# Kernel tuning notes

Measured on AMD Instinct MI355X. Metric: run time of the kernel, lower is better.

The kernel has to match this reference:

```python
import jax, jax.numpy as jnp
import numpy as np

D = 1024        # model dim
H = 8           # num heads
HD = D // H     # head dim = 128
EPS = 1e-6
B, L = 2, 4096


def _rmsnorm(x, g):
    # RMSNorm over the full model dim (applied before head split, as in source)
    return x * jax.lax.rsqrt(jnp.mean(x * x, axis=-1, keepdims=True) + EPS) * g


def _rope_interleaved(x, cos, sin):
    # x: [B, L, H, HD]; cos/sin: [L, HD//2]
    x1 = x[..., 0::2]
    x2 = x[..., 1::2]
    c = cos[None, :, None, :]
    s = sin[None, :, None, :]
    # interleave (x1*c - x2*s, x1*s + x2*c) back into even/odd lanes
    out = jnp.stack([x1 * c - x2 * s, x1 * s + x2 * c], axis=-1)
    return out.reshape(x.shape)


def setup_inputs() -> dict:
    key = jax.random.key(0)
    ks = jax.random.split(key, 6)
    x = jax.random.normal(ks[0], (B, L, D), dtype=jnp.float32)
    freqs_cos = jax.random.uniform(ks[1], (L, HD // 2), dtype=jnp.float32)
    freqs_sin = jax.random.uniform(ks[2], (L, HD // 2), dtype=jnp.float32)
    s = 1.0 / np.sqrt(D).astype(np.float32)
    w_qkv = jax.random.normal(ks[3], (D, 3 * D), dtype=jnp.float32) * s
    b_qkv = jnp.zeros((3 * D,), dtype=jnp.float32)
    g_q = jnp.ones((D,), dtype=jnp.float32)
    g_k = jnp.ones((D,), dtype=jnp.float32)
    w_out = jax.random.normal(ks[4], (D, D), dtype=jnp.float32) * s
    b_out = jnp.zeros((D,), dtype=jnp.float32)
    return {"x": x, "freqs_cos": freqs_cos, "freqs_sin": freqs_sin,
            "w_qkv": w_qkv, "b_qkv": b_qkv, "g_q": g_q, "g_k": g_k,
            "w_out": w_out, "b_out": b_out}


def reference(x, freqs_cos, freqs_sin, w_qkv, b_qkv, g_q, g_k, w_out, b_out):
    Bx, Lx, _ = x.shape
    qkv = x @ w_qkv + b_qkv                      # [B, L, 3D]
    q, k, v = jnp.split(qkv, 3, axis=-1)          # each [B, L, D]
    q = _rmsnorm(q, g_q)
    k = _rmsnorm(k, g_k)
    q = q.reshape(Bx, Lx, H, HD)
    k = k.reshape(Bx, Lx, H, HD)
    v = v.reshape(Bx, Lx, H, HD)
    q = _rope_interleaved(q, freqs_cos, freqs_sin)
    k = _rope_interleaved(k, freqs_cos, freqs_sin)
    scale = 1.0 / np.sqrt(HD)
    scores = jnp.einsum('blhd,bmhd->bhlm', q, k) * scale
    attn = jax.nn.softmax(scores, axis=-1)
    o = jnp.einsum('bhlm,bmhd->blhd', attn, v).reshape(Bx, Lx, D)
    return o @ w_out + b_out
```

## Files before the change

kernel.cpp:

```cpp
#include <hip/hip_runtime.h>
#include <hip/hip_bf16.h>
#include <stdint.h>

typedef __attribute__((ext_vector_type(8))) short short8;
typedef __attribute__((ext_vector_type(4))) short short4v;
typedef __attribute__((ext_vector_type(4))) float f32x4;
typedef __attribute__((ext_vector_type(16))) float f32x16;

#define LSEQ 4096
#define DMODEL 1024
#define NHEAD 8
#define HDIM 128
#define MTOT 8192
#define NQKV 3072

__device__ __forceinline__ unsigned short f2bf(float f){
  unsigned u = __float_as_uint(f);
  u += 0x7fffu + ((u >> 16) & 1u);
  return (unsigned short)(u >> 16);
}
__device__ __forceinline__ float bf2f(unsigned short h){
  return __uint_as_float(((unsigned)h) << 16);
}

typedef const __attribute__((address_space(1))) void* gas_ptr;
typedef __attribute__((address_space(3))) void* las_ptr;
__device__ __forceinline__ void gload_lds16(const void* g, void* l){
  __builtin_amdgcn_global_load_lds((gas_ptr)(uintptr_t)g,
                                   (las_ptr)(unsigned)(uintptr_t)l, 16, 0, 0);
}

__global__ __launch_bounds__(256) void k_cvt(const float* __restrict__ in,
                                             unsigned short* __restrict__ out, int n8){
  int i = blockIdx.x*256 + threadIdx.x;
  if (i >= n8) return;
  const float4* p = (const float4*)in + (size_t)i*2;
  float4 a = p[0], b = p[1];
  short8 r;
  r[0]=(short)f2bf(a.x); r[1]=(short)f2bf(a.y); r[2]=(short)f2bf(a.z); r[3]=(short)f2bf(a.w);
  r[4]=(short)f2bf(b.x); r[5]=(short)f2bf(b.y); r[6]=(short)f2bf(b.z); r[7]=(short)f2bf(b.w);
  *(short8*)(out + (size_t)i*8) = r;
}

__global__ __launch_bounds__(256) void k_transpose_cvt(const float* __restrict__ in,
                                                       unsigned short* __restrict__ out,
                                                       int R, int C){
  __shared__ unsigned short tile[32][33];
  int c0 = blockIdx.x*32, r0 = blockIdx.y*32;
  int tx = threadIdx.x & 31, ty = threadIdx.x >> 5;
  #pragma unroll
  for (int i=0;i<32;i+=8)
    tile[ty+i][tx] = f2bf(in[(size_t)(r0+ty+i)*C + c0+tx]);
  __syncthreads();
  #pragma unroll
  for (int i=0;i<32;i+=8)
    out[(size_t)(c0+ty+i)*R + r0+tx] = tile[tx][ty+i];
}

__global__ __launch_bounds__(256) void k_vT(const unsigned short* __restrict__ qkv,
                                            unsigned short* __restrict__ vT){
  __shared__ unsigned short tile[32][33];
  int bh = blockIdx.z; int b = bh >> 3, h = bh & 7;
  int l0 = blockIdx.x*32, d0 = blockIdx.y*32;
  const unsigned short* src = qkv + (size_t)b*LSEQ*NQKV + 2*DMODEL + h*HDIM;
  int tx = threadIdx.x & 31, ty = threadIdx.x >> 5;
  #pragma unroll
  for (int i=0;i<32;i+=8)
    tile[ty+i][tx] = src[(size_t)(l0+ty+i)*NQKV + d0+tx];
  __syncthreads();
  unsigned short* dst = vT + ((size_t)bh*HDIM + d0)*LSEQ + l0;
  #pragma unroll
  for (int i=0;i<32;i+=8)
    dst[(size_t)(ty+i)*LSEQ + tx] = tile[tx][ty+i];
}

template<int OUT_BF16>
__global__ __launch_bounds__(256) void k_gemm_bt(const unsigned short* __restrict__ A,
                                                 const unsigned short* __restrict__ Bt,
                                                 const float* __restrict__ bias,
                                                 void* __restrict__ Cout,
                                                 int M, int N, int K){
  __shared__ unsigned short As[128*64];
  __shared__ unsigned short Bs[128*64];
  int tid = threadIdx.x, lane = tid & 63, wave = tid >> 6;
  int wm = wave >> 1, wn = wave & 1;
  int nbx = N >> 7;
  int nwg = nbx * (M >> 7);
  int id  = blockIdx.y * nbx + blockIdx.x;
  int cpx = nwg >> 3;
  int swz = (id & 7) * cpx + (id >> 3);
  int m0 = (swz / nbx) * 128, n0 = (swz % nbx) * 128;
  f32x4 zero = {0.f,0.f,0.f,0.f};
  f32x4 acc[4][4];
  #pragma unroll
  for (int mi=0;mi<4;++mi)
    #pragma unroll
    for (int ni=0;ni<4;++ni) acc[mi][ni] = zero;

  int srow = lane >> 3;
  int soffb = (lane & 7) * 16;
  int scol = (soffb ^ (srow << 4)) >> 1;
  int cg = lane >> 4, cl = lane & 15;

  int nkt = K >> 6;
  for (int kt = 0; kt < nkt; ++kt){
    if (kt) __syncthreads();
    int kbase = kt*64;
    #pragma unroll
    for (int j=0;j<4;++j){
      int ch = wave*4 + j;
      int row = ch*8 + srow;
      gload_lds16(A  + (size_t)(m0+row)*K + kbase + scol, (char*)As + ch*1024);
      gload_lds16(Bt + (size_t)(n0+row)*K + kbase + scol, (char*)Bs + ch*1024);
    }
    __syncthreads();

    short8 af[4][2], bf[4][2];
    #pragma unroll
    for (int mi=0;mi<4;++mi){
      int row = wm*64 + mi*16 + cl;
      int key = (row & 7) << 4;
      #pragma unroll
      for (int kk=0;kk<2;++kk)
        af[mi][kk] = *(const short8*)((const char*)As + row*128 + ((kk*64 + cg*16) ^ key));
    }
    #pragma unroll
    for (int ni=0;ni<4;++ni){
      int row = wn*64 + ni*16 + cl;
      int key = (row & 7) << 4;
      #pragma unroll
      for (int kk=0;kk<2;++kk)
        bf[ni][kk] = *(const short8*)((const char*)Bs + row*128 + ((kk*64 + cg*16) ^ key));
    }
    #pragma unroll
    for (int kk=0;kk<2;++kk)
      #pragma unroll
      for (int mi=0;mi<4;++mi)
        #pragma unroll
        for (int ni=0;ni<4;++ni)
          acc[mi][ni] = __builtin_amdgcn_mfma_f32_16x16x32_bf16(af[mi][kk], bf[ni][kk], acc[mi][ni], 0,0,0);
  }

  #pragma unroll
  for (int ni=0;ni<4;++ni){
    int col = n0 + wn*64 + ni*16 + cl;
    float bv = bias[col];
    #pragma unroll
    for (int mi=0;mi<4;++mi){
      int r = m0 + wm*64 + mi*16 + cg*4;
      #pragma unroll
      for (int i=0;i<4;++i){
        float v = acc[mi][ni][i] + bv;
        if (OUT_BF16) ((unsigned short*)Cout)[(size_t)(r+i)*N + col] = f2bf(v);
        else          ((float*)Cout)[(size_t)(r+i)*N + col] = v;
      }
    }
  }
}

__global__ __launch_bounds__(256) void k_norm_rope(unsigned short* __restrict__ qkv,
                                                   const float* __restrict__ fcos,
                                                   const float* __restrict__ fsin,
                                                   const float* __restrict__ gq,
                                                   const float* __restrict__ gk){
  int bl = blockIdx.x;
  int l = bl & (LSEQ-1);
  int t = threadIdx.x;
  unsigned short* row = qkv + (size_t)bl * NQKV;
  int d0 = t*4;
  short4v qv = *(short4v*)(row + d0);
  short4v kv = *(short4v*)(row + DMODEL + d0);
  float q[4], k[4];
  #pragma unroll
  for (int j=0;j<4;++j){ q[j] = bf2f((unsigned short)qv[j]); k[j] = bf2f((unsigned short)kv[j]); }
  float sq = q[0]*q[0]+q[1]*q[1]+q[2]*q[2]+q[3]*q[3];
  float sk = k[0]*k[0]+k[1]*k[1]+k[2]*k[2]+k[3]*k[3];
  #pragma unroll
  for (int o=32;o;o>>=1){ sq += __shfl_xor(sq,o); sk += __shfl_xor(sk,o); }
  __shared__ float red[8];
  int lane = t & 63, wv = t >> 6;
  if (!lane){ red[wv] = sq; red[4+wv] = sk; }
  __syncthreads();
  sq = red[0]+red[1]+red[2]+red[3];
  sk = red[4]+red[5]+red[6]+red[7];
  const float K2 = 0.12753568849800323f;
  float rq = rsqrtf(sq*(1.f/1024.f) + 1e-6f);
  float rk = rsqrtf(sk*(1.f/1024.f) + 1e-6f) * K2;
  int hd = d0 & (HDIM-1);
  int fi = (l << 6) + (hd >> 1);
  float c0 = fcos[fi], s0 = fsin[fi], c1 = fcos[fi+1], s1 = fsin[fi+1];
  {
    float x1 = q[0]*rq*gq[d0],   x2 = q[1]*rq*gq[d0+1];
    float x3 = q[2]*rq*gq[d0+2], x4 = q[3]*rq*gq[d0+3];
    short4v qo;
    qo[0]=(short)f2bf(x1*c0 - x2*s0); qo[1]=(short)f2bf(x1*s0 + x2*c0);
    qo[2]=(short)f2bf(x3*c1 - x4*s1); qo[3]=(short)f2bf(x3*s1 + x4*c1);
    *(short4v*)(row + d0) = qo;
  }
  {
    float x1 = k[0]*rk*gk[d0],   x2 = k[1]*rk*gk[d0+1];
    float x3 = k[2]*rk*gk[d0+2], x4 = k[3]*rk*gk[d0+3];
    short4v ko;
    ko[0]=(short)f2bf(x1*c0 - x2*s0); ko[1]=(short)f2bf(x1*s0 + x2*c0);
    ko[2]=(short)f2bf(x3*c1 - x4*s1); ko[3]=(short)f2bf(x3*s1 + x4*c1);
    *(short4v*)(row + DMODEL + d0) = ko;
  }
}

__global__ __launch_bounds__(256, 2) void k_attn(const unsigned short* __restrict__ qkv,
                                                 const unsigned short* __restrict__ vT,
                                                 unsigned short* __restrict__ o){
  __shared__ unsigned short Ks[2][64*128];
  __shared__ unsigned short VTs[2][128*64];
  int bh = blockIdx.y; int b = bh >> 3, h = bh & 7;
  int q0 = blockIdx.x * 128;
  int tid = threadIdx.x, lane = tid & 63, wave = tid >> 6;
  int ql = lane & 31, hf = lane >> 5;
  const unsigned short* base = qkv + (size_t)b*LSEQ*NQKV + h*HDIM;
  const unsigned short* kgl = base + DMODEL;
  const unsigned short* vtg = vT + (size_t)bh*HDIM*LSEQ;

  short8 qf[8];
  {
    const unsigned short* qr = base + (size_t)(q0 + wave*32 + ql)*NQKV + hf*8;
    #pragma unroll
    for (int st=0;st<8;++st) qf[st] = *(const short8*)(qr + st*16);
  }
  short8 ones;
  #pragma unroll
  for (int j=0;j<8;++j) ones[j] = (short)0x3F80;

  f32x16 z16 = {0.f};
  f32x16 acc[4];
  acc[0]=z16; acc[1]=z16; acc[2]=z16; acc[3]=z16;
  f32x16 accl = z16;

  int key = (ql & 7) << 4;

  int v_dl   = lane >> 3;
  int v_srcb = ((lane & 7)*16) ^ (v_dl << 4);
  int cgk = (lane >> 4) & 3;

  const unsigned short* kptr[4];
  const unsigned short* vptr[4];
  #pragma unroll
  for (int j=0;j<4;++j){
    int ch = wave*4 + j;
    int row = ch*4 + cgk;
    int srcb = ((lane & 15)*16) ^ ((row & 7) << 4);
    kptr[j] = kgl + (size_t)row*NQKV + (srcb >> 1);
    int d = ch*8 + v_dl;
    vptr[j] = vtg + (size_t)d*LSEQ + (v_srcb >> 1);
    gload_lds16(kptr[j], (char*)Ks[0] + ch*1024);
    gload_lds16(vptr[j], (char*)VTs[0] + ch*1024);
    kptr[j] += 64*NQKV;
    vptr[j] += 64;
  }

  const int NT = LSEQ/64;
  for (int t = 0; t < NT; ++t){
    int cur = t & 1;
    __syncthreads();

    if (t+1 < NT){
      #pragma unroll
      for (int j=0;j<4;++j){
        int ch = wave*4 + j;
        gload_lds16(kptr[j], (char*)Ks[cur^1] + ch*1024);
        gload_lds16(vptr[j], (char*)VTs[cur^1] + ch*1024);
        kptr[j] += 64*NQKV;
        vptr[j] += 64;
      }
    }

    const char* kb = (const char*)Ks[cur];
    const char* vb = (const char*)VTs[cur];

    __builtin_amdgcn_s_setprio(1);
    f32x16 s0 = z16, s1 = z16;
    #pragma unroll
    for (int st=0;st<8;++st){
      int col = (hf*16 + st*32) ^ key;
      short8 kf0 = *(const short8*)(kb + ql*256 + col);
      s0 = __builtin_amdgcn_mfma_f32_32x32x16_bf16(kf0, qf[st], s0, 0,0,0);
    }
    #pragma unroll
    for (int st=0;st<8;++st){
      int col = (hf*16 + st*32) ^ key;
      short8 kf1 = *(const short8*)(kb + ql*256 + 8192 + col);
      s1 = __builtin_amdgcn_mfma_f32_32x32x16_bf16(kf1, qf[st], s1, 0,0,0);
      s0[2*st]   = __builtin_amdgcn_exp2f(s0[2*st]);
      s0[2*st+1] = __builtin_amdgcn_exp2f(s0[2*st+1]);
    }
    #pragma unroll
    for (int c=0;c<2;++c){
      unsigned c01, c23, c45, c67;
      int rb = c*8;
      asm("v_cvt_pk_bf16_f32 %0, %1, %2" : "=v"(c01) : "v"(s0[rb+0]), "v"(s0[rb+1]));
      asm("v_cvt_pk_bf16_f32 %0, %1, %2" : "=v"(c23) : "v"(s0[rb+2]), "v"(s0[rb+3]));
      asm("v_cvt_pk_bf16_f32 %0, %1, %2" : "=v"(c45) : "v"(s0[rb+4]), "v"(s0[rb+5]));
      asm("v_cvt_pk_bf16_f32 %0, %1, %2" : "=v"(c67) : "v"(s0[rb+6]), "v"(s0[rb+7]));
      asm("v_permlane32_swap_b32 %0, %1" : "+v"(c01), "+v"(c45));
      asm("v_permlane32_swap_b32 %0, %1" : "+v"(c23), "+v"(c67));
      union { unsigned u[4]; short8 v; } pu;
      pu.u[0] = c01; pu.u[1] = c23; pu.u[2] = c45; pu.u[3] = c67;
      short8 pa = pu.v;
      s1[rb+0] = __builtin_amdgcn_exp2f(s1[rb+0]);
      s1[rb+1] = __builtin_amdgcn_exp2f(s1[rb+1]);
      s1[rb+2] = __builtin_amdgcn_exp2f(s1[rb+2]);
      s1[rb+3] = __builtin_amdgcn_exp2f(s1[rb+3]);
      s1[rb+4] = __builtin_amdgcn_exp2f(s1[rb+4]);
      s1[rb+5] = __builtin_amdgcn_exp2f(s1[rb+5]);
      s1[rb+6] = __builtin_amdgcn_exp2f(s1[rb+6]);
      s1[rb+7] = __builtin_amdgcn_exp2f(s1[rb+7]);
      accl = __builtin_amdgcn_mfma_f32_32x32x16_bf16(pa, ones, accl, 0,0,0);
      #pragma unroll
      for (int dt=0;dt<4;++dt){
        int col = (c*32 + hf*16) ^ key;
        short8 vf = *(const short8*)(vb + (dt*32 + ql)*128 + col);
        acc[dt] = __builtin_amdgcn_mfma_f32_32x32x16_bf16(pa, vf, acc[dt], 0,0,0);
      }
    }
    #pragma unroll
    for (int c=2;c<4;++c){
      unsigned c01, c23, c45, c67;
      int rb = (c&1)*8;
      asm("v_cvt_pk_bf16_f32 %0, %1, %2" : "=v"(c01) : "v"(s1[rb+0]), "v"(s1[rb+1]));
      asm("v_cvt_pk_bf16_f32 %0, %1, %2" : "=v"(c23) : "v"(s1[rb+2]), "v"(s1[rb+3]));
      asm("v_cvt_pk_bf16_f32 %0, %1, %2" : "=v"(c45) : "v"(s1[rb+4]), "v"(s1[rb+5]));
      asm("v_cvt_pk_bf16_f32 %0, %1, %2" : "=v"(c67) : "v"(s1[rb+6]), "v"(s1[rb+7]));
      asm("v_permlane32_swap_b32 %0, %1" : "+v"(c01), "+v"(c45));
      asm("v_permlane32_swap_b32 %0, %1" : "+v"(c23), "+v"(c67));
      union { unsigned u[4]; short8 v; } pu;
      pu.u[0] = c01; pu.u[1] = c23; pu.u[2] = c45; pu.u[3] = c67;
      short8 pa = pu.v;
      accl = __builtin_amdgcn_mfma_f32_32x32x16_bf16(pa, ones, accl, 0,0,0);
      #pragma unroll
      for (int dt=0;dt<4;++dt){
        int col = (c*32 + hf*16) ^ key;
        short8 vf = *(const short8*)(vb + (dt*32 + ql)*128 + col);
        acc[dt] = __builtin_amdgcn_mfma_f32_32x32x16_bf16(pa, vf, acc[dt], 0,0,0);
      }
    }
    __builtin_amdgcn_s_setprio(0);
  }

  float rr[16];
  #pragma unroll
  for (int r=0;r<16;++r) rr[r] = __builtin_amdgcn_rcpf(accl[r]);
  size_t qbase = (size_t)(b*LSEQ + q0 + wave*32);
  #pragma unroll
  for (int dt=0;dt<4;++dt){
    int col = h*HDIM + dt*32 + ql;
    #pragma unroll
    for (int r=0;r<16;++r){
      int qrow = (r&3) + 8*(r>>2) + 4*hf;
      o[(qbase + qrow)*DMODEL + col] = f2bf(acc[dt][r]*rr[r]);
    }
  }
}

extern "C" void kernel_launch(void* const* d_in, const int* in_sizes, int n_in,
                              void* d_out, int out_size, void* d_ws, size_t ws_size,
                              hipStream_t stream) {
  const float* x    = (const float*)d_in[0];
  const float* fcos = (const float*)d_in[1];
  const float* fsin = (const float*)d_in[2];
  const float* wqkv = (const float*)d_in[3];
  const float* bqkv = (const float*)d_in[4];
  const float* gq   = (const float*)d_in[5];
  const float* gk   = (const float*)d_in[6];
  const float* wout = (const float*)d_in[7];
  const float* bout = (const float*)d_in[8];
  float* out = (float*)d_out;

  char* ws = (char*)d_ws;
  unsigned short* xb    = (unsigned short*)(ws);
  unsigned short* qkv   = (unsigned short*)(ws + (16ull<<20));
  unsigned short* ob    = (unsigned short*)(ws + (64ull<<20));
  unsigned short* wqkvT = (unsigned short*)(ws + (80ull<<20));
  unsigned short* woutT = (unsigned short*)(ws + (86ull<<20));
  unsigned short* vT    = xb;

  k_cvt<<<4096, 256, 0, stream>>>(x, xb, (MTOT*DMODEL)/8);
  k_transpose_cvt<<<dim3(96,32), 256, 0, stream>>>(wqkv, wqkvT, DMODEL, NQKV);
  k_transpose_cvt<<<dim3(32,32), 256, 0, stream>>>(wout, woutT, DMODEL, DMODEL);
  k_gemm_bt<1><<<dim3(NQKV/128, MTOT/128), 256, 0, stream>>>(xb, wqkvT, bqkv, qkv, MTOT, NQKV, DMODEL);
  k_norm_rope<<<MTOT, 256, 0, stream>>>(qkv, fcos, fsin, gq, gk);
  k_vT<<<dim3(LSEQ/32, HDIM/32, 16), 256, 0, stream>>>(qkv, vT);
  k_attn<<<dim3(LSEQ/128, 16), 256, 0, stream>>>(qkv, vT, ob);
  k_gemm_bt<0><<<dim3(DMODEL/128, MTOT/128), 256, 0, stream>>>(ob, woutT, bout, out, MTOT, DMODEL, DMODEL);
}
```

Measured before the change: 259.6 us.

## Double-buffer GEMM LDS tiles with 256x128 blocks of 8 waves

Replaces the 128x128 single-buffered GEMM with a 256x128 tile run by 512 threads. A and B tiles are double-buffered in LDS, and the next K-slice is prefetched while the current one is computed, using explicit vmcnt waits and barriers. MFMA sections get a raised wave priority. The aim is to hide global-load latency and halve the B-tile reloads per output row. In exchange, LDS use rises to 96KB and occupancy drops to one block per CU, and the out-projection grid shrinks to 256 blocks.

```diff
diff --git a/kernel.cpp b/kernel.cpp
--- a/kernel.cpp
+++ b/kernel.cpp
@@ -75,21 +75,22 @@
 }
 
 template<int OUT_BF16>
-__global__ __launch_bounds__(256) void k_gemm_bt(const unsigned short* __restrict__ A,
-                                                 const unsigned short* __restrict__ Bt,
-                                                 const float* __restrict__ bias,
-                                                 void* __restrict__ Cout,
-                                                 int M, int N, int K){
-  __shared__ unsigned short As[128*64];
-  __shared__ unsigned short Bs[128*64];
+__global__ __launch_bounds__(512, 1) void k_gemm256(const unsigned short* __restrict__ A,
+                                                    const unsigned short* __restrict__ Bt,
+                                                    const float* __restrict__ bias,
+                                                    void* __restrict__ Cout,
+                                                    int M, int N, int K){
+  __shared__ unsigned short As[2][256*64];
+  __shared__ unsigned short Bs[2][128*64];
   int tid = threadIdx.x, lane = tid & 63, wave = tid >> 6;
   int wm = wave >> 1, wn = wave & 1;
   int nbx = N >> 7;
-  int nwg = nbx * (M >> 7);
+  int nwg = nbx * (M >> 8);
   int id  = blockIdx.y * nbx + blockIdx.x;
   int cpx = nwg >> 3;
   int swz = (id & 7) * cpx + (id >> 3);
-  int m0 = (swz / nbx) * 128, n0 = (swz % nbx) * 128;
+  int m0 = (swz / nbx) * 256, n0 = (swz % nbx) * 128;
+
   f32x4 zero = {0.f,0.f,0.f,0.f};
   f32x4 acc[4][4];
   #pragma unroll
@@ -98,23 +99,51 @@
     for (int ni=0;ni<4;++ni) acc[mi][ni] = zero;
 
   int srow = lane >> 3;
-  int soffb = (lane & 7) * 16;
-  int scol = (soffb ^ (srow << 4)) >> 1;
+  int scol = (((lane & 7)*16) ^ (srow << 4)) >> 1;
   int cg = lane >> 4, cl = lane & 15;
 
-  int nkt = K >> 6;
-  for (int kt = 0; kt < nkt; ++kt){
-    if (kt) __syncthreads();
-    int kbase = kt*64;
-    #pragma unroll
-    for (int j=0;j<4;++j){
-      int ch = wave*4 + j;
-      int row = ch*8 + srow;
-      gload_lds16(A  + (size_t)(m0+row)*K + kbase + scol, (char*)As + ch*1024);
-      gload_lds16(Bt + (size_t)(n0+row)*K + kbase + scol, (char*)Bs + ch*1024);
-    }
-    __syncthreads();
-
+  const int NT2 = K >> 6;
+  #pragma unroll
+  for (int j=0;j<4;++j){
+    int ch = wave*4 + j;
+    int row = ch*8 + srow;
+    gload_lds16(A + (size_t)(m0+row)*K + scol, (char*)As[0] + ch*1024);
+  }
+  #pragma unroll
+  for (int j=0;j<2;++j){
+    int ch = wave*2 + j;
+    int row = ch*8 + srow;
+    gload_lds16(Bt + (size_t)(n0+row)*K + scol, (char*)Bs[0] + ch*1024);
+  }
+
+  for (int kt = 0; kt < NT2; ++kt){
+    int cur = kt & 1;
+    __builtin_amdgcn_s_barrier();
+    __builtin_amdgcn_sched_barrier(0);
+    if (kt+1 < NT2){
+      int kbase = (kt+1)*64;
+      #pragma unroll
+      for (int j=0;j<4;++j){
+        int ch = wave*4 + j;
+        int row = ch*8 + srow;
+        gload_lds16(A + (size_t)(m0+row)*K + kbase + scol, (char*)As[cur^1] + ch*1024);
+      }
+      #pragma unroll
+      for (int j=0;j<2;++j){
+        int ch = wave*2 + j;
+        int row = ch*8 + srow;
+        gload_lds16(Bt + (size_t)(n0+row)*K + kbase + scol, (char*)Bs[cur^1] + ch*1024);
+      }
+      asm volatile("s_waitcnt vmcnt(6)" ::: "memory");
+    } else {
+      asm volatile("s_waitcnt vmcnt(0)" ::: "memory");
+    }
+    __builtin_amdgcn_sched_barrier(0);
+    __builtin_amdgcn_s_barrier();
+    __builtin_amdgcn_sched_barrier(0);
+
+    const char* ab = (const char*)As[cur];
+    const char* bb = (const char*)Bs[cur];
     short8 af[4][2], bf[4][2];
     #pragma unroll
     for (int mi=0;mi<4;++mi){
@@ -122,7 +151,7 @@
       int key = (row & 7) << 4;
       #pragma unroll
       for (int kk=0;kk<2;++kk)
-        af[mi][kk] = *(const short8*)((const char*)As + row*128 + ((kk*64 + cg*16) ^ key));
+        af[mi][kk] = *(const short8*)(ab + row*128 + ((kk*64 + cg*16) ^ key));
     }
     #pragma unroll
     for (int ni=0;ni<4;++ni){
@@ -130,8 +159,9 @@
       int key = (row & 7) << 4;
       #pragma unroll
       for (int kk=0;kk<2;++kk)
-        bf[ni][kk] = *(const short8*)((const char*)Bs + row*128 + ((kk*64 + cg*16) ^ key));
-    }
+        bf[ni][kk] = *(const short8*)(bb + row*128 + ((kk*64 + cg*16) ^ key));
+    }
+    __builtin_amdgcn_s_setprio(1);
     #pragma unroll
     for (int kk=0;kk<2;++kk)
       #pragma unroll
@@ -139,6 +169,7 @@
         #pragma unroll
         for (int ni=0;ni<4;++ni)
           acc[mi][ni] = __builtin_amdgcn_mfma_f32_16x16x32_bf16(af[mi][kk], bf[ni][kk], acc[mi][ni], 0,0,0);
+    __builtin_amdgcn_s_setprio(0);
   }
 
   #pragma unroll
@@ -385,9 +416,9 @@
   k_cvt<<<4096, 256, 0, stream>>>(x, xb, (MTOT*DMODEL)/8);
   k_transpose_cvt<<<dim3(96,32), 256, 0, stream>>>(wqkv, wqkvT, DMODEL, NQKV);
   k_transpose_cvt<<<dim3(32,32), 256, 0, stream>>>(wout, woutT, DMODEL, DMODEL);
-  k_gemm_bt<1><<<dim3(NQKV/128, MTOT/128), 256, 0, stream>>>(xb, wqkvT, bqkv, qkv, MTOT, NQKV, DMODEL);
+  k_gemm256<1><<<dim3(NQKV/128, MTOT/256), 512, 0, stream>>>(xb, wqkvT, bqkv, qkv, MTOT, NQKV, DMODEL);
   k_norm_rope<<<MTOT, 256, 0, stream>>>(qkv, fcos, fsin, gq, gk);
   k_vT<<<dim3(LSEQ/32, HDIM/32, 16), 256, 0, stream>>>(qkv, vT);
   k_attn<<<dim3(LSEQ/128, 16), 256, 0, stream>>>(qkv, vT, ob);
-  k_gemm_bt<0><<<dim3(DMODEL/128, MTOT/128), 256, 0, stream>>>(ob, woutT, bout, out, MTOT, DMODEL, DMODEL);
-}
+  k_gemm256<0><<<dim3(DMODEL/128, MTOT/256), 512, 0, stream>>>(ob, woutT, bout, out, MTOT, DMODEL, DMODEL);
+}
```

Result: slower. 267.9 us (+3.2%).
